# Kernel optimization log

Hardware: AMD Instinct MI355X
Metric: run time of the kernel (lower is better)

## Reference

```python
import jax, jax.numpy as jnp
import numpy as np

N, E = 50000, 800000
DIN, H, DOUT, L = 128, 128, 64, 3
NEG_SLOPE = 0.2  # PyG GATConv default


def setup_inputs() -> dict:
    key = jax.random.key(0)
    ks = jax.random.split(key, 12)
    s = lambda i, shape: (jax.random.normal(ks[i], shape, jnp.float32) * 0.05)
    return {
        "x": jax.random.normal(ks[0], (N, DIN), jnp.float32),
        "edge_index": jax.random.randint(ks[1], (2, E), 0, N, jnp.int64 if jax.config.jax_enable_x64 else jnp.int32),
        "W_emb": s(2, (DIN, H)), "b_emb": jnp.zeros((H,), jnp.float32),
        "gat_W": s(3, (L, H, H)), "gat_as": s(4, (L, H)), "gat_ad": s(5, (L, H)),
        "gat_b": jnp.zeros((L, H), jnp.float32),
        "Wn1": s(6, (H, H)), "bn1": jnp.zeros((H,), jnp.float32),
        "Wn2": s(7, (H, DOUT)), "bn2": jnp.zeros((DOUT,), jnp.float32),
        "We1": s(8, (2 * H, H)), "be1": jnp.zeros((H,), jnp.float32),
        "We2": s(9, (H, 3)), "be2": jnp.zeros((3,), jnp.float32),
    }


def _gat_layer(h, src, dst, n, W, a_src, a_dst, b):
    # Single-head GATConv (PyG defaults: heads=1, concat, self-loops already in src/dst)
    xw = h @ W                                   # [N, H]
    alpha_s = xw @ a_src                          # [N]
    alpha_d = xw @ a_dst                          # [N]
    logits = jax.nn.leaky_relu(alpha_s[src] + alpha_d[dst], NEG_SLOPE)  # [E']
    m = jax.ops.segment_max(logits, dst, num_segments=n)
    p = jnp.exp(logits - m[dst])
    denom = jax.ops.segment_sum(p, dst, num_segments=n)
    alpha = p / denom[dst]                        # softmax over incoming edges
    return jax.ops.segment_sum(alpha[:, None] * xw[src], dst, num_segments=n) + b


def reference(x, edge_index, W_emb, b_emb, gat_W, gat_as, gat_ad, gat_b,
              Wn1, bn1, Wn2, bn2, We1, be1, We2, be2):
    n = x.shape[0]
    src0, dst0 = edge_index[0], edge_index[1]
    loops = jnp.arange(n, dtype=src0.dtype)
    src = jnp.concatenate([src0, loops])          # GATConv adds self-loops by default
    dst = jnp.concatenate([dst0, loops])

    h = jax.nn.relu(x @ W_emb + b_emb)            # dropout off (eval mode)
    for l in range(L):
        h_new = _gat_layer(h, src, dst, n, gat_W[l], gat_as[l], gat_ad[l], gat_b[l])
        h = jax.nn.relu(h + h_new)                # residual + relu

    node_pred = jax.nn.relu(h @ Wn1 + bn1) @ Wn2 + bn2            # [N, DOUT]
    ef = jnp.concatenate([h[src0], h[dst0]], axis=1)              # vectorized edge gather [E, 2H]
    edge_pred = jax.nn.relu(ef @ We1 + be1) @ We2 + be2           # [E, 3]
    graph_emb = jnp.mean(h, axis=0, keepdims=True)                # batch=None path [1, H]
    return node_pred, edge_pred, graph_emb
```

## Files before the change

kernel.cpp:

```cpp
#include <hip/hip_runtime.h>

#define NNODES 50000
#define NEDGES 800000
#define HDIM 128
#define DOUT 64
#define NLAYERS 3
#define NEG_SLOPE 0.2f

#define NODE_OUT_ELEMS (NNODES * DOUT)
#define EDGE_OUT_ELEMS (NEDGES * 3)
#define GEMB_OFF (NODE_OUT_ELEMS + EDGE_OUT_ELEMS)

typedef __attribute__((ext_vector_type(8))) short short8;
typedef __attribute__((ext_vector_type(4))) float f32x4;
typedef unsigned long long u64;

__device__ __forceinline__ float bf2f(unsigned short u) {
    union { unsigned int i; float f; } v; v.i = ((unsigned int)u) << 16; return v.f;
}
__device__ __forceinline__ unsigned short f2bf(float f) {
    union { unsigned int i; float f; } v; v.f = f;
    unsigned int b = v.i;
    unsigned int r = (b + 0x7FFFu + ((b >> 16) & 1u)) >> 16;
    return (unsigned short)r;
}
__device__ __forceinline__ float leaky(float x) { return x > 0.f ? x : NEG_SLOPE * x; }
__device__ __forceinline__ float wread(const void* p, size_t i, int f32) {
    return f32 ? ((const float*)p)[i] : bf2f(((const unsigned short*)p)[i]);
}

__device__ __forceinline__ int eget(const int* e32, const int* iflag, int which, int e) {
    int idx = which * NEDGES + e;
    return (*iflag) ? e32[idx] : e32[2 * idx];
}

__global__ void init_kernel(int* cnt, int* cur, float* gsum, int* flags) {
    int i = blockIdx.x * 256 + threadIdx.x;
    if (i < NNODES) { cnt[i] = 0; cur[i] = 0; }
    if (blockIdx.x == 0) {
        if (threadIdx.x < HDIM) gsum[threadIdx.x] = 0.f;
        if (threadIdx.x < 2) flags[threadIdx.x] = 0;
    }
}

__global__ void detect_kernel(const unsigned short* xb, const int* e32,
                              int* fflag, int* iflag) {
    if (blockIdx.x == 0) {
        int hit = 0;
        for (int j = threadIdx.x; j < 4096; j += 256) {
            int e = (xb[j] >> 7) & 0xFF;
            if (e >= 0x90) hit = 1;
        }
        if (hit) atomicOr(fflag, 1);
    } else {
        int hit = 0;
        for (int t = threadIdx.x; t < 16384; t += 256) {
            int i = t * 48;
            if (e32[2 * i + 1] != 0) hit = 1;
        }
        if (__any(hit)) {
            if ((threadIdx.x & 63) == 0) atomicOr(iflag, 1);
        }
    }
}

__global__ __launch_bounds__(256) void gemm_mfma_kernel(
    const void* __restrict__ Av, int a_from_x, const void* __restrict__ Bw,
    size_t b_off, const void* __restrict__ bias, unsigned short* __restrict__ C,
    int M, int relu, const int* __restrict__ f32flag,
    float* __restrict__ alpha_s, float* __restrict__ alpha_d,
    const void* __restrict__ gat_as, const void* __restrict__ gat_ad, int aoff)
{
    constexpr int KP = 128 + 8;
    __shared__ unsigned short sA[64 * KP];
    __shared__ float pS[64][4], pD[64][4];
    const int f32 = *f32flag;
    const int tid = threadIdx.x;
    const int row0 = blockIdx.x * 64;

    if (a_from_x && f32) {
        const float* Af = (const float*)Av;
        for (int c = tid; c < 64 * 16; c += 256) {
            int r = c >> 4, cp = c & 15;
            int gr = row0 + r;
            unsigned short o[8] = {0, 0, 0, 0, 0, 0, 0, 0};
            if (gr < M) {
                float4 v0 = *(const float4*)(Af + (size_t)gr * 128 + cp * 8);
                float4 v1 = *(const float4*)(Af + (size_t)gr * 128 + cp * 8 + 4);
                o[0] = f2bf(v0.x); o[1] = f2bf(v0.y); o[2] = f2bf(v0.z); o[3] = f2bf(v0.w);
                o[4] = f2bf(v1.x); o[5] = f2bf(v1.y); o[6] = f2bf(v1.z); o[7] = f2bf(v1.w);
            }
            *(uint4*)(&sA[r * KP + cp * 8]) = *(uint4*)o;
        }
    } else {
        const unsigned short* A = (const unsigned short*)Av;
        for (int c = tid; c < 64 * 16; c += 256) {
            int r = c >> 4, cp = c & 15;
            int gr = row0 + r;
            uint4 v = {0u, 0u, 0u, 0u};
            if (gr < M) v = *(const uint4*)(A + (size_t)gr * 128 + cp * 8);
            *(uint4*)(&sA[r * KP + cp * 8]) = v;
        }
    }
    __syncthreads();

    const int wave = tid >> 6, lane = tid & 63;
    const int quad = lane >> 4, l15 = lane & 15;
    const int ncol0 = wave * 32;

    short8 bw[4][2];
    #pragma unroll
    for (int kk = 0; kk < 4; kk++)
        #pragma unroll
        for (int nt = 0; nt < 2; nt++) {
            int n = ncol0 + nt * 16 + l15;
            short8 t;
            #pragma unroll
            for (int j = 0; j < 8; j++)
                t[j] = (short)f2bf(wread(Bw, b_off + (size_t)(kk * 32 + quad * 8 + j) * 128 + n, f32));
            bw[kk][nt] = t;
        }

    float bv[2];
    #pragma unroll
    for (int nt = 0; nt < 2; nt++)
        bv[nt] = bias ? wread(bias, ncol0 + nt * 16 + l15, f32) : 0.f;

    f32x4 acc[4][2];
    #pragma unroll
    for (int mt = 0; mt < 4; mt++)
        #pragma unroll
        for (int nt = 0; nt < 2; nt++) {
            acc[mt][nt][0] = bv[nt]; acc[mt][nt][1] = bv[nt];
            acc[mt][nt][2] = bv[nt]; acc[mt][nt][3] = bv[nt];
        }

    #pragma unroll
    for (int kk = 0; kk < 4; kk++) {
        short8 a[4];
        #pragma unroll
        for (int mt = 0; mt < 4; mt++)
            a[mt] = *(const short8*)(&sA[(mt * 16 + l15) * KP + kk * 32 + quad * 8]);
        #pragma unroll
        for (int mt = 0; mt < 4; mt++)
            #pragma unroll
            for (int nt = 0; nt < 2; nt++)
                acc[mt][nt] = __builtin_amdgcn_mfma_f32_16x16x32_bf16(
                    a[mt], bw[kk][nt], acc[mt][nt], 0, 0, 0);
    }

    if (alpha_s) {
        float as0 = wread(gat_as, (size_t)aoff + ncol0 + l15, f32);
        float as1 = wread(gat_as, (size_t)aoff + ncol0 + 16 + l15, f32);
        float ad0 = wread(gat_ad, (size_t)aoff + ncol0 + l15, f32);
        float ad1 = wread(gat_ad, (size_t)aoff + ncol0 + 16 + l15, f32);
        #pragma unroll
        for (int mt = 0; mt < 4; mt++)
            #pragma unroll
            for (int q = 0; q < 4; q++) {
                float vs = acc[mt][0][q] * as0 + acc[mt][1][q] * as1;
                float vd = acc[mt][0][q] * ad0 + acc[mt][1][q] * ad1;
                #pragma unroll
                for (int d = 1; d < 16; d <<= 1) {
                    vs += __shfl_xor(vs, d);
                    vd += __shfl_xor(vd, d);
                }
                if (l15 == 0) {
                    int r = mt * 16 + quad * 4 + q;
                    pS[r][wave] = vs; pD[r][wave] = vd;
                }
            }
        __syncthreads();
        if (tid < 64) {
            int row = row0 + tid;
            if (row < M) {
                alpha_s[row] = pS[tid][0] + pS[tid][1] + pS[tid][2] + pS[tid][3];
                alpha_d[row] = pD[tid][0] + pD[tid][1] + pD[tid][2] + pD[tid][3];
            }
        }
    }

    #pragma unroll
    for (int mt = 0; mt < 4; mt++)
        #pragma unroll
        for (int nt = 0; nt < 2; nt++)
            #pragma unroll
            for (int q = 0; q < 4; q++) {
                int row = row0 + mt * 16 + quad * 4 + q;
                if (row < M) {
                    float v = acc[mt][nt][q];
                    if (relu) v = fmaxf(v, 0.f);
                    C[(size_t)row * 128 + ncol0 + nt * 16 + l15] = f2bf(v);
                }
            }
}

__global__ __launch_bounds__(256) void node_mlp_kernel(
    const unsigned short* __restrict__ h, const void* __restrict__ Wn1,
    const void* __restrict__ bn1, const void* __restrict__ Wn2,
    const void* __restrict__ bn2, float* __restrict__ out,
    float* __restrict__ gsum, int M, const int* __restrict__ f32flag)
{
    constexpr int KP = 128 + 8;
    __shared__ unsigned short sA[64 * KP];
    const int f32 = *f32flag;
    const int tid = threadIdx.x;
    const int row0 = blockIdx.x * 64;

    for (int c = tid; c < 64 * 16; c += 256) {
        int r = c >> 4, cp = c & 15;
        int gr = row0 + r;
        uint4 v = {0u, 0u, 0u, 0u};
        if (gr < M) v = *(const uint4*)(h + (size_t)gr * 128 + cp * 8);
        *(uint4*)(&sA[r * KP + cp * 8]) = v;
    }
    __syncthreads();

    if (tid < 128) {
        float hs = 0.f;
        for (int r = 0; r < 64; r++) hs += bf2f(sA[r * KP + tid]);
        atomicAdd(&gsum[tid], hs);
    }

    const int wave = tid >> 6, lane = tid & 63;
    const int quad = lane >> 4, l15 = lane & 15;
    const int ncol0 = wave * 32;

    {
        short8 bw[4][2];
        #pragma unroll
        for (int kk = 0; kk < 4; kk++)
            #pragma unroll
            for (int nt = 0; nt < 2; nt++) {
                int n = ncol0 + nt * 16 + l15;
                short8 t;
                #pragma unroll
                for (int j = 0; j < 8; j++)
                    t[j] = (short)f2bf(wread(Wn1, (size_t)(kk * 32 + quad * 8 + j) * 128 + n, f32));
                bw[kk][nt] = t;
            }
        float bv[2];
        #pragma unroll
        for (int nt = 0; nt < 2; nt++)
            bv[nt] = wread(bn1, ncol0 + nt * 16 + l15, f32);

        f32x4 acc[4][2];
        #pragma unroll
        for (int mt = 0; mt < 4; mt++)
            #pragma unroll
            for (int nt = 0; nt < 2; nt++) {
                acc[mt][nt][0] = bv[nt]; acc[mt][nt][1] = bv[nt];
                acc[mt][nt][2] = bv[nt]; acc[mt][nt][3] = bv[nt];
            }
        #pragma unroll
        for (int kk = 0; kk < 4; kk++) {
            short8 a[4];
            #pragma unroll
            for (int mt = 0; mt < 4; mt++)
                a[mt] = *(const short8*)(&sA[(mt * 16 + l15) * KP + kk * 32 + quad * 8]);
            #pragma unroll
            for (int mt = 0; mt < 4; mt++)
                #pragma unroll
                for (int nt = 0; nt < 2; nt++)
                    acc[mt][nt] = __builtin_amdgcn_mfma_f32_16x16x32_bf16(
                        a[mt], bw[kk][nt], acc[mt][nt], 0, 0, 0);
        }
        __syncthreads();
        #pragma unroll
        for (int mt = 0; mt < 4; mt++)
            #pragma unroll
            for (int nt = 0; nt < 2; nt++)
                #pragma unroll
                for (int q = 0; q < 4; q++) {
                    int r = mt * 16 + quad * 4 + q;
                    sA[r * KP + ncol0 + nt * 16 + l15] =
                        f2bf(fmaxf(acc[mt][nt][q], 0.f));
                }
        __syncthreads();
    }

    {
        const int col = wave * 16 + l15;
        short8 bw[4];
        #pragma unroll
        for (int kk = 0; kk < 4; kk++) {
            short8 t;
            #pragma unroll
            for (int j = 0; j < 8; j++)
                t[j] = (short)f2bf(wread(Wn2, (size_t)(kk * 32 + quad * 8 + j) * 64 + col, f32));
            bw[kk] = t;
        }
        float bv = wread(bn2, col, f32);
        f32x4 acc[4];
        #pragma unroll
        for (int mt = 0; mt < 4; mt++) {
            acc[mt][0] = bv; acc[mt][1] = bv; acc[mt][2] = bv; acc[mt][3] = bv;
        }
        #pragma unroll
        for (int kk = 0; kk < 4; kk++) {
            short8 a[4];
            #pragma unroll
            for (int mt = 0; mt < 4; mt++)
                a[mt] = *(const short8*)(&sA[(mt * 16 + l15) * KP + kk * 32 + quad * 8]);
            #pragma unroll
            for (int mt = 0; mt < 4; mt++)
                acc[mt] = __builtin_amdgcn_mfma_f32_16x16x32_bf16(
                    a[mt], bw[kk], acc[mt], 0, 0, 0);
        }
        #pragma unroll
        for (int mt = 0; mt < 4; mt++)
            #pragma unroll
            for (int q = 0; q < 4; q++) {
                int row = row0 + mt * 16 + quad * 4 + q;
                if (row < M) out[(size_t)row * 64 + col] = acc[mt][q];
            }
    }
}

__global__ __launch_bounds__(256) void edge_ab_kernel(
    const unsigned short* __restrict__ h, const void* __restrict__ We1,
    const void* __restrict__ be1, unsigned short* __restrict__ Axw,
    unsigned short* __restrict__ Bh, int M, const int* __restrict__ f32flag)
{
    constexpr int KP = 128 + 8;
    __shared__ unsigned short sA[64 * KP];
    const int f32 = *f32flag;
    const int tid = threadIdx.x;
    const int row0 = blockIdx.x * 64;

    for (int c = tid; c < 64 * 16; c += 256) {
        int r = c >> 4, cp = c & 15;
        int gr = row0 + r;
        uint4 v = {0u, 0u, 0u, 0u};
        if (gr < M) v = *(const uint4*)(h + (size_t)gr * 128 + cp * 8);
        *(uint4*)(&sA[r * KP + cp * 8]) = v;
    }
    __syncthreads();

    const int wave = tid >> 6, lane = tid & 63;
    const int quad = lane >> 4, l15 = lane & 15;
    const int ncol0 = wave * 32;

    #pragma unroll
    for (int half = 0; half < 2; half++) {
        const size_t b_off = (size_t)half * 128 * 128;
        unsigned short* Cp = half ? Bh : Axw;

        short8 bw[4][2];
        #pragma unroll
        for (int kk = 0; kk < 4; kk++)
            #pragma unroll
            for (int nt = 0; nt < 2; nt++) {
                int n = ncol0 + nt * 16 + l15;
                short8 t;
                #pragma unroll
                for (int j = 0; j < 8; j++)
                    t[j] = (short)f2bf(wread(We1, b_off + (size_t)(kk * 32 + quad * 8 + j) * 128 + n, f32));
                bw[kk][nt] = t;
            }
        float bv[2];
        #pragma unroll
        for (int nt = 0; nt < 2; nt++)
            bv[nt] = half ? 0.f : wread(be1, ncol0 + nt * 16 + l15, f32);

        f32x4 acc[4][2];
        #pragma unroll
        for (int mt = 0; mt < 4; mt++)
            #pragma unroll
            for (int nt = 0; nt < 2; nt++) {
                acc[mt][nt][0] = bv[nt]; acc[mt][nt][1] = bv[nt];
                acc[mt][nt][2] = bv[nt]; acc[mt][nt][3] = bv[nt];
            }
        #pragma unroll
        for (int kk = 0; kk < 4; kk++) {
            short8 a[4];
            #pragma unroll
            for (int mt = 0; mt < 4; mt++)
                a[mt] = *(const short8*)(&sA[(mt * 16 + l15) * KP + kk * 32 + quad * 8]);
            #pragma unroll
            for (int mt = 0; mt < 4; mt++)
                #pragma unroll
                for (int nt = 0; nt < 2; nt++)
                    acc[mt][nt] = __builtin_amdgcn_mfma_f32_16x16x32_bf16(
                        a[mt], bw[kk][nt], acc[mt][nt], 0, 0, 0);
        }
        #pragma unroll
        for (int mt = 0; mt < 4; mt++)
            #pragma unroll
            for (int nt = 0; nt < 2; nt++)
                #pragma unroll
                for (int q = 0; q < 4; q++) {
                    int row = row0 + mt * 16 + quad * 4 + q;
                    if (row < M)
                        Cp[(size_t)row * 128 + ncol0 + nt * 16 + l15] =
                            f2bf(acc[mt][nt][q]);
                }
    }
}

__global__ void count_kernel(const int* e32, const int* iflag, int* cnt) {
    int e = blockIdx.x * 256 + threadIdx.x;
    if (e < NEDGES) atomicAdd(&cnt[eget(e32, iflag, 1, e)], 1);
}
__global__ void scan1_kernel(const int* cnt, int* off, int* bsum) {
    __shared__ int s[256];
    int t = threadIdx.x, i = blockIdx.x * 256 + t;
    int v = (i < NNODES) ? cnt[i] : 0;
    s[t] = v;
    __syncthreads();
    for (int d = 1; d < 256; d <<= 1) {
        int add = (t >= d) ? s[t - d] : 0;
        __syncthreads();
        s[t] += add;
        __syncthreads();
    }
    if (i < NNODES) off[i] = s[t] - v;
    if (t == 255) bsum[blockIdx.x] = s[255];
}
__global__ void scan2_kernel(int* bsum, int nblk) {
    if (threadIdx.x == 0 && blockIdx.x == 0) {
        int run = 0;
        for (int c = 0; c < nblk; c++) { int t = bsum[c]; bsum[c] = run; run += t; }
    }
}
__global__ void scan3_kernel(int* off, const int* bsum) {
    int i = blockIdx.x * 256 + threadIdx.x;
    if (i < NNODES) off[i] += bsum[blockIdx.x];
}
__global__ void fill_kernel(const int* e32, const int* iflag, const int* off,
                            int* cur, u64* csrp, int use_pack) {
    int e = blockIdx.x * 256 + threadIdx.x;
    if (e < NEDGES) {
        int s = eget(e32, iflag, 0, e);
        int d = eget(e32, iflag, 1, e);
        int p = atomicAdd(&cur[d], 1);
        int pos = off[d] + p;
        if (use_pack)
            csrp[pos] = (u64)s | ((u64)d << 17) | ((u64)e << 34);
        else
            ((int*)csrp)[pos] = s;
    }
}

__global__ void aggregate_kernel(const unsigned short* __restrict__ xw,
                                 const float* __restrict__ as_, const float* __restrict__ ad_,
                                 const int* __restrict__ off, const u64* __restrict__ csrp,
                                 int use_pack, const void* __restrict__ gat_b, int boff,
                                 unsigned short* __restrict__ h,
                                 const int* __restrict__ f32flag) {
    const int f32 = *f32flag;
    int wave = threadIdx.x >> 6, lane = threadIdx.x & 63;
    int n = blockIdx.x * 4 + wave;
    if (n >= NNODES) return;
    int o0 = off[n];
    int o1 = (n == NNODES - 1) ? NEDGES : off[n + 1];
    int deg = o1 - o0;
    float adn = ad_[n];
    float lself = leaky(as_[n] + adn);

    int deg64 = deg < 64 ? deg : 64;
    int idxv = 0; float av = 0.f;
    if (lane < deg64) {
        idxv = use_pack ? (int)(csrp[o0 + lane] & 0x1FFFF)
                        : ((const int*)csrp)[o0 + lane];
        av = as_[idxv];
    }

    float m = lself;
    if (lane < deg64) m = fmaxf(m, leaky(av + adn));
    for (int i = 64 + lane; i < deg; i += 64) {
        int s = use_pack ? (int)(csrp[o0 + i] & 0x1FFFF)
                         : ((const int*)csrp)[o0 + i];
        m = fmaxf(m, leaky(as_[s] + adn));
    }
    #pragma unroll
    for (int d = 32; d >= 1; d >>= 1) m = fmaxf(m, __shfl_xor(m, d));

    const int slot = lane >> 4;
    const int l15  = lane & 15;
    float denom = 0.f;
    float acc[8];
    #pragma unroll
    for (int k = 0; k < 8; k++) acc[k] = 0.f;

    int i0 = slot, i1 = slot + 4;
    int sidx0 = __shfl(idxv, i0 & 63);
    float aval0 = __shfl(av, i0 & 63);
    int sidx1 = __shfl(idxv, i1 & 63);
    float aval1 = __shfl(av, i1 & 63);
    uint4 rv0 = {0u, 0u, 0u, 0u}, rv1 = {0u, 0u, 0u, 0u};
    if (i0 < deg64) rv0 = *(const uint4*)(xw + (size_t)sidx0 * HDIM + l15 * 8);
    if (i1 < deg64) rv1 = *(const uint4*)(xw + (size_t)sidx1 * HDIM + l15 * 8);
    for (int t0 = 0; t0 < deg64; t0 += 4) {
        int i2 = i0 + 8;
        int sidx2 = __shfl(idxv, i2 & 63);
        float aval2 = __shfl(av, i2 & 63);
        uint4 rv2 = {0u, 0u, 0u, 0u};
        if (i2 < deg64)
            rv2 = *(const uint4*)(xw + (size_t)sidx2 * HDIM + l15 * 8);
        if (i0 < deg64) {
            float p = __expf(leaky(aval0 + adn) - m);
            denom += p;
            const unsigned short* rp = (const unsigned short*)&rv0;
            #pragma unroll
            for (int k = 0; k < 8; k++) acc[k] += p * bf2f(rp[k]);
        }
        i0 = i1; aval0 = aval1; rv0 = rv1;
        i1 = i2; aval1 = aval2; rv1 = rv2;
    }
    for (int i = 64 + slot; i < deg; i += 4) {
        int s = use_pack ? (int)(csrp[o0 + i] & 0x1FFFF)
                         : ((const int*)csrp)[o0 + i];
        float p = __expf(leaky(as_[s] + adn) - m);
        denom += p;
        uint4 rv = *(const uint4*)(xw + (size_t)s * HDIM + l15 * 8);
        const unsigned short* rp = (const unsigned short*)&rv;
        #pragma unroll
        for (int k = 0; k < 8; k++) acc[k] += p * bf2f(rp[k]);
    }

    #pragma unroll
    for (int d = 16; d <= 32; d <<= 1) {
        denom += __shfl_xor(denom, d);
        #pragma unroll
        for (int k = 0; k < 8; k++) acc[k] += __shfl_xor(acc[k], d);
    }

    float ps = __expf(lself - m);
    denom += ps;
    uint4 sv = *(const uint4*)(xw + (size_t)n * HDIM + l15 * 8);
    const unsigned short* sp = (const unsigned short*)&sv;
    #pragma unroll
    for (int k = 0; k < 8; k++) acc[k] += ps * bf2f(sp[k]);

    if (slot == 0) {
        float inv = 1.f / denom;
        size_t base = (size_t)n * HDIM + l15 * 8;
        uint4 hv = *(const uint4*)(h + base);
        const unsigned short* hp = (const unsigned short*)&hv;
        unsigned short outv[8];
        #pragma unroll
        for (int k = 0; k < 8; k++) {
            float hx = bf2f(hp[k]);
            float bx = wread(gat_b, boff + l15 * 8 + k, f32);
            outv[k] = f2bf(fmaxf(hx + acc[k] * inv + bx, 0.f));
        }
        *(uint4*)(h + base) = *(uint4*)outv;
    }
}

__global__ __launch_bounds__(256) void edge_split_kernel(
    const unsigned short* __restrict__ A, const unsigned short* __restrict__ B,
    const int* __restrict__ e32, const int* __restrict__ iflag,
    const u64* __restrict__ csrp, int use_pack,
    const void* __restrict__ We2, const void* __restrict__ be2,
    float* __restrict__ eout, const int* __restrict__ f32flag)
{
    const int f32 = *f32flag;
    const int lane = threadIdx.x & 63;
    const int slot = lane >> 4, l15 = lane & 15;

    float w2[8][3];
    #pragma unroll
    for (int j = 0; j < 8; j++)
        #pragma unroll
        for (int c = 0; c < 3; c++)
            w2[j][c] = wread(We2, (l15 * 8 + j) * 3 + c, f32);
    const float bo0 = wread(be2, 0, f32);
    const float bo1 = wread(be2, 1, f32);
    const float bo2 = wread(be2, 2, f32);

    const int gw = (blockIdx.x * 256 + threadIdx.x) >> 6;
    const int stride = gridDim.x * 32;
    for (int e0 = gw * 8 + slot * 2; e0 < NEDGES; e0 += stride) {
        const int e1 = e0 + 1;
        const bool has1 = (e1 < NEDGES);
        int s0, d0, oe0, s1 = 0, d1 = 0, oe1 = 0;
        if (use_pack) {
            u64 pk0 = csrp[e0];
            s0 = (int)(pk0 & 0x1FFFF); d0 = (int)((pk0 >> 17) & 0x1FFFF);
            oe0 = (int)(pk0 >> 34);
            if (has1) {
                u64 pk1 = csrp[e1];
                s1 = (int)(pk1 & 0x1FFFF); d1 = (int)((pk1 >> 17) & 0x1FFFF);
                oe1 = (int)(pk1 >> 34);
            }
        } else {
            s0 = eget(e32, iflag, 0, e0); d0 = eget(e32, iflag, 1, e0); oe0 = e0;
            if (has1) {
                s1 = eget(e32, iflag, 0, e1); d1 = eget(e32, iflag, 1, e1); oe1 = e1;
            }
        }
        uint4 a0 = *(const uint4*)(A + (size_t)s0 * HDIM + l15 * 8);
        uint4 b0 = *(const uint4*)(B + (size_t)d0 * HDIM + l15 * 8);
        uint4 a1 = {0u, 0u, 0u, 0u}, b1 = {0u, 0u, 0u, 0u};
        if (has1) {
            a1 = *(const uint4*)(A + (size_t)s1 * HDIM + l15 * 8);
            b1 = *(const uint4*)(B + (size_t)d1 * HDIM + l15 * 8);
        }
        const unsigned short* ap0 = (const unsigned short*)&a0;
        const unsigned short* bp0 = (const unsigned short*)&b0;
        const unsigned short* ap1 = (const unsigned short*)&a1;
        const unsigned short* bp1 = (const unsigned short*)&b1;
        float s00 = 0.f, s01 = 0.f, s02 = 0.f;
        float s10 = 0.f, s11 = 0.f, s12 = 0.f;
        #pragma unroll
        for (int j = 0; j < 8; j++) {
            float v0 = fmaxf(bf2f(ap0[j]) + bf2f(bp0[j]), 0.f);
            float v1 = fmaxf(bf2f(ap1[j]) + bf2f(bp1[j]), 0.f);
            s00 += v0 * w2[j][0]; s01 += v0 * w2[j][1]; s02 += v0 * w2[j][2];
            s10 += v1 * w2[j][0]; s11 += v1 * w2[j][1]; s12 += v1 * w2[j][2];
        }
        #pragma unroll
        for (int dd = 1; dd < 16; dd <<= 1) {
            s00 += __shfl_xor(s00, dd); s01 += __shfl_xor(s01, dd); s02 += __shfl_xor(s02, dd);
            s10 += __shfl_xor(s10, dd); s11 += __shfl_xor(s11, dd); s12 += __shfl_xor(s12, dd);
        }
        if (l15 == 0) {
            eout[(size_t)oe0 * 3 + 0] = s00 + bo0;
            eout[(size_t)oe0 * 3 + 1] = s01 + bo1;
            eout[(size_t)oe0 * 3 + 2] = s02 + bo2;
            if (has1) {
                eout[(size_t)oe1 * 3 + 0] = s10 + bo0;
                eout[(size_t)oe1 * 3 + 1] = s11 + bo1;
                eout[(size_t)oe1 * 3 + 2] = s12 + bo2;
            }
        }
    }
}

__global__ void gout_kernel(const float* gsum, float* out) {
    int f = threadIdx.x;
    out[GEMB_OFF + f] = gsum[f] * (1.f / (float)NNODES);
}

extern "C" __attribute__((visibility("default")))
void kernel_launch(void* const* d_in, const int* in_sizes, int n_in,
                   void* d_out, int out_size, void* d_ws, size_t ws_size,
                   hipStream_t stream) {
    const void* x      = d_in[0];
    const int*  eidx   = (const int*)d_in[1];
    const void* W_emb  = d_in[2];
    const void* b_emb  = d_in[3];
    const void* gat_W  = d_in[4];
    const void* gat_as = d_in[5];
    const void* gat_ad = d_in[6];
    const void* gat_b  = d_in[7];
    const void* Wn1    = d_in[8];
    const void* bn1    = d_in[9];
    const void* Wn2    = d_in[10];
    const void* bn2    = d_in[11];
    const void* We1    = d_in[12];
    const void* be1    = d_in[13];
    const void* We2    = d_in[14];
    const void* be2    = d_in[15];
    float* out = (float*)d_out;

    char* ws = (char*)d_ws;
    unsigned short* h       = (unsigned short*)(ws);
    unsigned short* xw      = (unsigned short*)(ws + 12800000);
    float*          alpha_s = (float*)(ws + 25600000);
    float*          alpha_d = (float*)(ws + 25800000);
    int*            cnt     = (int*)(ws + 26000000);
    int*            off     = (int*)(ws + 26200000);
    int*            bsum    = (int*)(ws + 26400000);
    float*          gsum    = (float*)(ws + 26401024);
    int*            iflag   = (int*)(ws + 26401536);
    int*            fflag   = (int*)(ws + 26401540);
    u64*            csrp    = (u64*)(ws + 26608000);
    int*            cur     = (int*)alpha_s;

    const int use_pack = (ws_size >= (size_t)33008000) ? 1 : 0;

    const int node_blks = (NNODES + 255) / 256;
    const int edge_blks = (NEDGES + 255) / 256;
    const int g64       = (NNODES + 63) / 64;

    init_kernel<<<node_blks, 256, 0, stream>>>(cnt, cur, gsum, iflag);
    detect_kernel<<<2, 256, 0, stream>>>((const unsigned short*)x, eidx, fflag, iflag);

    gemm_mfma_kernel<<<g64, 256, 0, stream>>>(
        x, 1, W_emb, 0, b_emb, h, NNODES, 1, fflag,
        (float*)0, (float*)0, (const void*)0, (const void*)0, 0);

    count_kernel<<<edge_blks, 256, 0, stream>>>(eidx, iflag, cnt);
    scan1_kernel<<<node_blks, 256, 0, stream>>>(cnt, off, bsum);
    scan2_kernel<<<1, 64, 0, stream>>>(bsum, node_blks);
    scan3_kernel<<<node_blks, 256, 0, stream>>>(off, bsum);
    fill_kernel<<<edge_blks, 256, 0, stream>>>(eidx, iflag, off, cur, csrp, use_pack);

    for (int l = 0; l < NLAYERS; l++) {
        gemm_mfma_kernel<<<g64, 256, 0, stream>>>(
            h, 0, gat_W, (size_t)l * HDIM * HDIM, (const void*)0, xw, NNODES, 0, fflag,
            alpha_s, alpha_d, gat_as, gat_ad, l * HDIM);
        aggregate_kernel<<<(NNODES + 3) / 4, 256, 0, stream>>>(
            xw, alpha_s, alpha_d, off, csrp, use_pack, gat_b, l * HDIM, h, fflag);
    }

    node_mlp_kernel<<<g64, 256, 0, stream>>>(
        h, Wn1, bn1, Wn2, bn2, out, gsum, NNODES, fflag);
    gout_kernel<<<1, 128, 0, stream>>>(gsum, out);

    edge_ab_kernel<<<g64, 256, 0, stream>>>(
        h, We1, be1, xw, h, NNODES, fflag);
    edge_split_kernel<<<2048, 256, 0, stream>>>(
        xw, h, eidx, iflag, csrp, use_pack, We2, be2,
        out + NODE_OUT_ELEMS, fflag);
}
```

Before: 542.7 us.

## Fuse node MLP with edge projection and software-pipeline edge gather loop

Merges the node MLP and the edge first-layer projection into one tail kernel, so each 64-row tile of h is loaded into shared memory once and one launch is removed. The edge output loop now prefetches the next iteration's indices and gathered rows while computing the current pair, to hide gather latency. Risks: Bh aliases h, so the tail kernel writes h in place while other blocks may still read their own tiles (each block only touches its own rows). The tail kernel also needs more registers, and the has1 guard is dropped on the assumption that the edge count is even.

```diff
diff --git a/kernel.cpp b/kernel.cpp
--- a/kernel.cpp
+++ b/kernel.cpp
@@ -195,11 +195,14 @@
             }
 }
 
-__global__ __launch_bounds__(256) void node_mlp_kernel(
-    const unsigned short* __restrict__ h, const void* __restrict__ Wn1,
-    const void* __restrict__ bn1, const void* __restrict__ Wn2,
-    const void* __restrict__ bn2, float* __restrict__ out,
-    float* __restrict__ gsum, int M, const int* __restrict__ f32flag)
+__global__ __launch_bounds__(256) void tail_kernel(
+    const unsigned short* __restrict__ h,
+    const void* __restrict__ We1, const void* __restrict__ be1,
+    unsigned short* __restrict__ Axw, unsigned short* __restrict__ Bh,
+    const void* __restrict__ Wn1, const void* __restrict__ bn1,
+    const void* __restrict__ Wn2, const void* __restrict__ bn2,
+    float* __restrict__ out, float* __restrict__ gsum,
+    int M, const int* __restrict__ f32flag)
 {
     constexpr int KP = 128 + 8;
     __shared__ unsigned short sA[64 * KP];
@@ -225,6 +228,62 @@
     const int wave = tid >> 6, lane = tid & 63;
     const int quad = lane >> 4, l15 = lane & 15;
     const int ncol0 = wave * 32;
+
+    #pragma unroll
+    for (int half = 0; half < 2; half++) {
+        const size_t b_off = (size_t)half * 128 * 128;
+        unsigned short* Cp = half ? Bh : Axw;
+
+        short8 bw[4][2];
+        #pragma unroll
+        for (int kk = 0; kk < 4; kk++)
+            #pragma unroll
+            for (int nt = 0; nt < 2; nt++) {
+                int n = ncol0 + nt * 16 + l15;
+                short8 t;
+                #pragma unroll
+                for (int j = 0; j < 8; j++)
+                    t[j] = (short)f2bf(wread(We1, b_off + (size_t)(kk * 32 + quad * 8 + j) * 128 + n, f32));
+                bw[kk][nt] = t;
+            }
+        float bv[2];
+        #pragma unroll
+        for (int nt = 0; nt < 2; nt++)
+            bv[nt] = half ? 0.f : wread(be1, ncol0 + nt * 16 + l15, f32);
+
+        f32x4 acc[4][2];
+        #pragma unroll
+        for (int mt = 0; mt < 4; mt++)
+            #pragma unroll
+            for (int nt = 0; nt < 2; nt++) {
+                acc[mt][nt][0] = bv[nt]; acc[mt][nt][1] = bv[nt];
+                acc[mt][nt][2] = bv[nt]; acc[mt][nt][3] = bv[nt];
+            }
+        #pragma unroll
+        for (int kk = 0; kk < 4; kk++) {
+            short8 a[4];
+            #pragma unroll
+            for (int mt = 0; mt < 4; mt++)
+                a[mt] = *(const short8*)(&sA[(mt * 16 + l15) * KP + kk * 32 + quad * 8]);
+            #pragma unroll
+            for (int mt = 0; mt < 4; mt++)
+                #pragma unroll
+                for (int nt = 0; nt < 2; nt++)
+                    acc[mt][nt] = __builtin_amdgcn_mfma_f32_16x16x32_bf16(
+                        a[mt], bw[kk][nt], acc[mt][nt], 0, 0, 0);
+        }
+        #pragma unroll
+        for (int mt = 0; mt < 4; mt++)
+            #pragma unroll
+            for (int nt = 0; nt < 2; nt++)
+                #pragma unroll
+                for (int q = 0; q < 4; q++) {
+                    int row = row0 + mt * 16 + quad * 4 + q;
+                    if (row < M)
+                        Cp[(size_t)row * 128 + ncol0 + nt * 16 + l15] =
+                            f2bf(acc[mt][nt][q]);
+                }
+    }
 
     {
         short8 bw[4][2];
@@ -314,87 +373,6 @@
                 int row = row0 + mt * 16 + quad * 4 + q;
                 if (row < M) out[(size_t)row * 64 + col] = acc[mt][q];
             }
-    }
-}
-
-__global__ __launch_bounds__(256) void edge_ab_kernel(
-    const unsigned short* __restrict__ h, const void* __restrict__ We1,
-    const void* __restrict__ be1, unsigned short* __restrict__ Axw,
-    unsigned short* __restrict__ Bh, int M, const int* __restrict__ f32flag)
-{
-    constexpr int KP = 128 + 8;
-    __shared__ unsigned short sA[64 * KP];
-    const int f32 = *f32flag;
-    const int tid = threadIdx.x;
-    const int row0 = blockIdx.x * 64;
-
-    for (int c = tid; c < 64 * 16; c += 256) {
-        int r = c >> 4, cp = c & 15;
-        int gr = row0 + r;
-        uint4 v = {0u, 0u, 0u, 0u};
-        if (gr < M) v = *(const uint4*)(h + (size_t)gr * 128 + cp * 8);
-        *(uint4*)(&sA[r * KP + cp * 8]) = v;
-    }
-    __syncthreads();
-
-    const int wave = tid >> 6, lane = tid & 63;
-    const int quad = lane >> 4, l15 = lane & 15;
-    const int ncol0 = wave * 32;
-
-    #pragma unroll
-    for (int half = 0; half < 2; half++) {
-        const size_t b_off = (size_t)half * 128 * 128;
-        unsigned short* Cp = half ? Bh : Axw;
-
-        short8 bw[4][2];
-        #pragma unroll
-        for (int kk = 0; kk < 4; kk++)
-            #pragma unroll
-            for (int nt = 0; nt < 2; nt++) {
-                int n = ncol0 + nt * 16 + l15;
-                short8 t;
-                #pragma unroll
-                for (int j = 0; j < 8; j++)
-                    t[j] = (short)f2bf(wread(We1, b_off + (size_t)(kk * 32 + quad * 8 + j) * 128 + n, f32));
-                bw[kk][nt] = t;
-            }
-        float bv[2];
-        #pragma unroll
-        for (int nt = 0; nt < 2; nt++)
-            bv[nt] = half ? 0.f : wread(be1, ncol0 + nt * 16 + l15, f32);
-
-        f32x4 acc[4][2];
-        #pragma unroll
-        for (int mt = 0; mt < 4; mt++)
-            #pragma unroll
-            for (int nt = 0; nt < 2; nt++) {
-                acc[mt][nt][0] = bv[nt]; acc[mt][nt][1] = bv[nt];
-                acc[mt][nt][2] = bv[nt]; acc[mt][nt][3] = bv[nt];
-            }
-        #pragma unroll
-        for (int kk = 0; kk < 4; kk++) {
-            short8 a[4];
-            #pragma unroll
-            for (int mt = 0; mt < 4; mt++)
-                a[mt] = *(const short8*)(&sA[(mt * 16 + l15) * KP + kk * 32 + quad * 8]);
-            #pragma unroll
-            for (int mt = 0; mt < 4; mt++)
-                #pragma unroll
-                for (int nt = 0; nt < 2; nt++)
-                    acc[mt][nt] = __builtin_amdgcn_mfma_f32_16x16x32_bf16(
-                        a[mt], bw[kk][nt], acc[mt][nt], 0, 0, 0);
-        }
-        #pragma unroll
-        for (int mt = 0; mt < 4; mt++)
-            #pragma unroll
-            for (int nt = 0; nt < 2; nt++)
-                #pragma unroll
-                for (int q = 0; q < 4; q++) {
-                    int row = row0 + mt * 16 + quad * 4 + q;
-                    if (row < M)
-                        Cp[(size_t)row * 128 + ncol0 + nt * 16 + l15] =
-                            f2bf(acc[mt][nt][q]);
-                }
     }
 }
 
@@ -572,36 +550,50 @@
 
     const int gw = (blockIdx.x * 256 + threadIdx.x) >> 6;
     const int stride = gridDim.x * 32;
-    for (int e0 = gw * 8 + slot * 2; e0 < NEDGES; e0 += stride) {
-        const int e1 = e0 + 1;
-        const bool has1 = (e1 < NEDGES);
-        int s0, d0, oe0, s1 = 0, d1 = 0, oe1 = 0;
+
+    int ec = gw * 8 + slot * 2;
+    int sc0 = 0, dc0 = 0, oc0 = 0, sc1 = 0, dc1 = 0, oc1 = 0;
+    uint4 ac0 = {0u,0u,0u,0u}, bc0 = {0u,0u,0u,0u};
+    uint4 ac1 = {0u,0u,0u,0u}, bc1 = {0u,0u,0u,0u};
+    if (ec < NEDGES) {
         if (use_pack) {
-            u64 pk0 = csrp[e0];
-            s0 = (int)(pk0 & 0x1FFFF); d0 = (int)((pk0 >> 17) & 0x1FFFF);
-            oe0 = (int)(pk0 >> 34);
-            if (has1) {
-                u64 pk1 = csrp[e1];
-                s1 = (int)(pk1 & 0x1FFFF); d1 = (int)((pk1 >> 17) & 0x1FFFF);
-                oe1 = (int)(pk1 >> 34);
-            }
+            u64 p0 = csrp[ec], p1 = csrp[ec + 1];
+            sc0 = (int)(p0 & 0x1FFFF); dc0 = (int)((p0 >> 17) & 0x1FFFF); oc0 = (int)(p0 >> 34);
+            sc1 = (int)(p1 & 0x1FFFF); dc1 = (int)((p1 >> 17) & 0x1FFFF); oc1 = (int)(p1 >> 34);
         } else {
-            s0 = eget(e32, iflag, 0, e0); d0 = eget(e32, iflag, 1, e0); oe0 = e0;
-            if (has1) {
-                s1 = eget(e32, iflag, 0, e1); d1 = eget(e32, iflag, 1, e1); oe1 = e1;
-            }
-        }
-        uint4 a0 = *(const uint4*)(A + (size_t)s0 * HDIM + l15 * 8);
-        uint4 b0 = *(const uint4*)(B + (size_t)d0 * HDIM + l15 * 8);
-        uint4 a1 = {0u, 0u, 0u, 0u}, b1 = {0u, 0u, 0u, 0u};
-        if (has1) {
-            a1 = *(const uint4*)(A + (size_t)s1 * HDIM + l15 * 8);
-            b1 = *(const uint4*)(B + (size_t)d1 * HDIM + l15 * 8);
-        }
-        const unsigned short* ap0 = (const unsigned short*)&a0;
-        const unsigned short* bp0 = (const unsigned short*)&b0;
-        const unsigned short* ap1 = (const unsigned short*)&a1;
-        const unsigned short* bp1 = (const unsigned short*)&b1;
+            sc0 = eget(e32, iflag, 0, ec);     dc0 = eget(e32, iflag, 1, ec);     oc0 = ec;
+            sc1 = eget(e32, iflag, 0, ec + 1); dc1 = eget(e32, iflag, 1, ec + 1); oc1 = ec + 1;
+        }
+        ac0 = *(const uint4*)(A + (size_t)sc0 * HDIM + l15 * 8);
+        bc0 = *(const uint4*)(B + (size_t)dc0 * HDIM + l15 * 8);
+        ac1 = *(const uint4*)(A + (size_t)sc1 * HDIM + l15 * 8);
+        bc1 = *(const uint4*)(B + (size_t)dc1 * HDIM + l15 * 8);
+    }
+
+    while (ec < NEDGES) {
+        const int en = ec + stride;
+        int sn0 = 0, dn0 = 0, on0 = 0, sn1 = 0, dn1 = 0, on1 = 0;
+        uint4 an0 = {0u,0u,0u,0u}, bn0 = {0u,0u,0u,0u};
+        uint4 an1 = {0u,0u,0u,0u}, bn1v = {0u,0u,0u,0u};
+        if (en < NEDGES) {
+            if (use_pack) {
+                u64 p0 = csrp[en], p1 = csrp[en + 1];
+                sn0 = (int)(p0 & 0x1FFFF); dn0 = (int)((p0 >> 17) & 0x1FFFF); on0 = (int)(p0 >> 34);
+                sn1 = (int)(p1 & 0x1FFFF); dn1 = (int)((p1 >> 17) & 0x1FFFF); on1 = (int)(p1 >> 34);
+            } else {
+                sn0 = eget(e32, iflag, 0, en);     dn0 = eget(e32, iflag, 1, en);     on0 = en;
+                sn1 = eget(e32, iflag, 0, en + 1); dn1 = eget(e32, iflag, 1, en + 1); on1 = en + 1;
+            }
+            an0 = *(const uint4*)(A + (size_t)sn0 * HDIM + l15 * 8);
+            bn0 = *(const uint4*)(B + (size_t)dn0 * HDIM + l15 * 8);
+            an1 = *(const uint4*)(A + (size_t)sn1 * HDIM + l15 * 8);
+            bn1v = *(const uint4*)(B + (size_t)dn1 * HDIM + l15 * 8);
+        }
+
+        const unsigned short* ap0 = (const unsigned short*)&ac0;
+        const unsigned short* bp0 = (const unsigned short*)&bc0;
+        const unsigned short* ap1 = (const unsigned short*)&ac1;
+        const unsigned short* bp1 = (const unsigned short*)&bc1;
         float s00 = 0.f, s01 = 0.f, s02 = 0.f;
         float s10 = 0.f, s11 = 0.f, s12 = 0.f;
         #pragma unroll
@@ -617,15 +609,17 @@
             s10 += __shfl_xor(s10, dd); s11 += __shfl_xor(s11, dd); s12 += __shfl_xor(s12, dd);
         }
         if (l15 == 0) {
-            eout[(size_t)oe0 * 3 + 0] = s00 + bo0;
-            eout[(size_t)oe0 * 3 + 1] = s01 + bo1;
-            eout[(size_t)oe0 * 3 + 2] = s02 + bo2;
-            if (has1) {
-                eout[(size_t)oe1 * 3 + 0] = s10 + bo0;
-                eout[(size_t)oe1 * 3 + 1] = s11 + bo1;
-                eout[(size_t)oe1 * 3 + 2] = s12 + bo2;
-            }
-        }
+            eout[(size_t)oc0 * 3 + 0] = s00 + bo0;
+            eout[(size_t)oc0 * 3 + 1] = s01 + bo1;
+            eout[(size_t)oc0 * 3 + 2] = s02 + bo2;
+            eout[(size_t)oc1 * 3 + 0] = s10 + bo0;
+            eout[(size_t)oc1 * 3 + 1] = s11 + bo1;
+            eout[(size_t)oc1 * 3 + 2] = s12 + bo2;
+        }
+
+        ec = en;
+        sc0 = sn0; dc0 = dn0; oc0 = on0; sc1 = sn1; dc1 = dn1; oc1 = on1;
+        ac0 = an0; bc0 = bn0; ac1 = an1; bc1 = bn1v;
     }
 }
 
@@ -697,12 +691,10 @@
             xw, alpha_s, alpha_d, off, csrp, use_pack, gat_b, l * HDIM, h, fflag);
     }
 
-    node_mlp_kernel<<<g64, 256, 0, stream>>>(
-        h, Wn1, bn1, Wn2, bn2, out, gsum, NNODES, fflag);
+    tail_kernel<<<g64, 256, 0, stream>>>(
+        h, We1, be1, xw, h, Wn1, bn1, Wn2, bn2, out, gsum, NNODES, fflag);
     gout_kernel<<<1, 128, 0, stream>>>(gsum, out);
 
-    edge_ab_kernel<<<g64, 256, 0, stream>>>(
-        h, We1, be1, xw, h, NNODES, fflag);
     edge_split_kernel<<<2048, 256, 0, stream>>>(
         xw, h, eidx, iflag, csrp, use_pack, We2, be2,
         out + NODE_OUT_ELEMS, fflag);
```

Measured after the change: 550.9 us. About the same (+1.5%).

## Bin edges into src/dst slice blocks for cache-local edge MLP gathers

Applied to the files above, without the earlier changes.

Before the edge MLP, edges are binned into an 8x8 grid of source/destination node slices. This uses a per-block histogram, a global scan and a scatter into a packed edge buffer. Each group of blocks in the edge split kernel then walks one source slice's eight bins, so the A and B row gathers stay within a small, cache-resident working set. The B projection is now written into the not-yet-used node output buffer instead of overwriting h, and the node MLP is moved after the edge MLP. In exchange the change adds five extra kernels and another pass over the edge list, and it only applies when the workspace is large enough.

```diff
diff --git a/kernel.cpp b/kernel.cpp
--- a/kernel.cpp
+++ b/kernel.cpp
@@ -6,6 +6,7 @@
 #define DOUT 64
 #define NLAYERS 3
 #define NEG_SLOPE 0.2f
+#define BSLICE 6250
 
 #define NODE_OUT_ELEMS (NNODES * DOUT)
 #define EDGE_OUT_ELEMS (NEDGES * 3)
@@ -28,7 +29,6 @@
 __device__ __forceinline__ float wread(const void* p, size_t i, int f32) {
     return f32 ? ((const float*)p)[i] : bf2f(((const unsigned short*)p)[i]);
 }
-
 __device__ __forceinline__ int eget(const int* e32, const int* iflag, int which, int e) {
     int idx = which * NEDGES + e;
     return (*iflag) ? e32[idx] : e32[2 * idx];
@@ -320,7 +320,7 @@
 __global__ __launch_bounds__(256) void edge_ab_kernel(
     const unsigned short* __restrict__ h, const void* __restrict__ We1,
     const void* __restrict__ be1, unsigned short* __restrict__ Axw,
-    unsigned short* __restrict__ Bh, int M, const int* __restrict__ f32flag)
+    unsigned short* __restrict__ Bsc, int M, const int* __restrict__ f32flag)
 {
     constexpr int KP = 128 + 8;
     __shared__ unsigned short sA[64 * KP];
@@ -344,7 +344,7 @@
     #pragma unroll
     for (int half = 0; half < 2; half++) {
         const size_t b_off = (size_t)half * 128 * 128;
-        unsigned short* Cp = half ? Bh : Axw;
+        unsigned short* Cp = half ? Bsc : Axw;
 
         short8 bw[4][2];
         #pragma unroll
@@ -440,6 +440,53 @@
         else
             ((int*)csrp)[pos] = s;
     }
+}
+
+__global__ void hist_kernel(const int* e32, const int* iflag, int* bcnt) {
+    __shared__ int hcnt[64];
+    int tid = threadIdx.x;
+    if (tid < 64) hcnt[tid] = 0;
+    __syncthreads();
+    int e = blockIdx.x * 256 + tid;
+    int s = eget(e32, iflag, 0, e);
+    int d = eget(e32, iflag, 1, e);
+    int b = (s / BSLICE) * 8 + (d / BSLICE);
+    atomicAdd(&hcnt[b], 1);
+    __syncthreads();
+    if (tid < 64) bcnt[tid * 3125 + blockIdx.x] = hcnt[tid];
+}
+__global__ void gscan1_kernel(int* a, int n, int* bs) {
+    __shared__ int s[256];
+    int t = threadIdx.x, i = blockIdx.x * 256 + t;
+    int v = (i < n) ? a[i] : 0;
+    s[t] = v;
+    __syncthreads();
+    for (int d = 1; d < 256; d <<= 1) {
+        int add = (t >= d) ? s[t - d] : 0;
+        __syncthreads();
+        s[t] += add;
+        __syncthreads();
+    }
+    if (i < n) a[i] = s[t] - v;
+    if (t == 255) bs[blockIdx.x] = s[255];
+}
+__global__ void gscan3_kernel(int* a, int n, const int* bs) {
+    int i = blockIdx.x * 256 + threadIdx.x;
+    if (i < n) a[i] += bs[blockIdx.x];
+}
+__global__ void scatter_kernel(const int* e32, const int* iflag,
+                               const int* bcnt, u64* csrb) {
+    __shared__ int curb[64];
+    int tid = threadIdx.x;
+    if (tid < 64) curb[tid] = 0;
+    __syncthreads();
+    int e = blockIdx.x * 256 + tid;
+    int s = eget(e32, iflag, 0, e);
+    int d = eget(e32, iflag, 1, e);
+    int b = (s / BSLICE) * 8 + (d / BSLICE);
+    int p = atomicAdd(&curb[b], 1);
+    int pos = bcnt[b * 3125 + blockIdx.x] + p;
+    csrb[pos] = (u64)s | ((u64)d << 17) | ((u64)e << 34);
 }
 
 __global__ void aggregate_kernel(const unsigned short* __restrict__ xw,
@@ -552,7 +599,7 @@
 __global__ __launch_bounds__(256) void edge_split_kernel(
     const unsigned short* __restrict__ A, const unsigned short* __restrict__ B,
     const int* __restrict__ e32, const int* __restrict__ iflag,
-    const u64* __restrict__ csrp, int use_pack,
+    const u64* __restrict__ csrb, const int* __restrict__ bcnt, int use_big,
     const void* __restrict__ We2, const void* __restrict__ be2,
     float* __restrict__ eout, const int* __restrict__ f32flag)
 {
@@ -570,27 +617,8 @@
     const float bo1 = wread(be2, 1, f32);
     const float bo2 = wread(be2, 2, f32);
 
-    const int gw = (blockIdx.x * 256 + threadIdx.x) >> 6;
-    const int stride = gridDim.x * 32;
-    for (int e0 = gw * 8 + slot * 2; e0 < NEDGES; e0 += stride) {
-        const int e1 = e0 + 1;
-        const bool has1 = (e1 < NEDGES);
-        int s0, d0, oe0, s1 = 0, d1 = 0, oe1 = 0;
-        if (use_pack) {
-            u64 pk0 = csrp[e0];
-            s0 = (int)(pk0 & 0x1FFFF); d0 = (int)((pk0 >> 17) & 0x1FFFF);
-            oe0 = (int)(pk0 >> 34);
-            if (has1) {
-                u64 pk1 = csrp[e1];
-                s1 = (int)(pk1 & 0x1FFFF); d1 = (int)((pk1 >> 17) & 0x1FFFF);
-                oe1 = (int)(pk1 >> 34);
-            }
-        } else {
-            s0 = eget(e32, iflag, 0, e0); d0 = eget(e32, iflag, 1, e0); oe0 = e0;
-            if (has1) {
-                s1 = eget(e32, iflag, 0, e1); d1 = eget(e32, iflag, 1, e1); oe1 = e1;
-            }
-        }
+    auto do_pair = [&](int s0, int d0, int oe0,
+                       int s1, int d1, int oe1, bool has1) {
         uint4 a0 = *(const uint4*)(A + (size_t)s0 * HDIM + l15 * 8);
         uint4 b0 = *(const uint4*)(B + (size_t)d0 * HDIM + l15 * 8);
         uint4 a1 = {0u, 0u, 0u, 0u}, b1 = {0u, 0u, 0u, 0u};
@@ -625,6 +653,46 @@
                 eout[(size_t)oe1 * 3 + 1] = s11 + bo1;
                 eout[(size_t)oe1 * 3 + 2] = s12 + bo2;
             }
+        }
+    };
+
+    if (use_big) {
+        const int kx = blockIdx.x & 7;
+        const int wloc = (blockIdx.x >> 3) * 4 + (threadIdx.x >> 6);
+        for (int j = 0; j < 8; j++) {
+            int b = kx * 8 + j;
+            int base = bcnt[b * 3125];
+            int end  = (b == 63) ? NEDGES : bcnt[(b + 1) * 3125];
+            for (int e0 = base + wloc * 8 + slot * 2; e0 < end; e0 += 1024 * 8) {
+                u64 p0 = csrb[e0];
+                int s0 = (int)(p0 & 0x1FFFF);
+                int d0 = (int)((p0 >> 17) & 0x1FFFF);
+                int o0 = (int)(p0 >> 34);
+                bool has1 = (e0 + 1 < end);
+                int s1 = 0, d1 = 0, o1 = 0;
+                if (has1) {
+                    u64 p1 = csrb[e0 + 1];
+                    s1 = (int)(p1 & 0x1FFFF);
+                    d1 = (int)((p1 >> 17) & 0x1FFFF);
+                    o1 = (int)(p1 >> 34);
+                }
+                do_pair(s0, d0, o0, s1, d1, o1, has1);
+            }
+        }
+    } else {
+        const int gw = (blockIdx.x * 256 + threadIdx.x) >> 6;
+        const int stride = gridDim.x * 32;
+        for (int e0 = gw * 8 + slot * 2; e0 < NEDGES; e0 += stride) {
+            int s0 = eget(e32, iflag, 0, e0);
+            int d0 = eget(e32, iflag, 1, e0);
+            bool has1 = (e0 + 1 < NEDGES);
+            int s1 = 0, d1 = 0, o1 = 0;
+            if (has1) {
+                s1 = eget(e32, iflag, 0, e0 + 1);
+                d1 = eget(e32, iflag, 1, e0 + 1);
+                o1 = e0 + 1;
+            }
+            do_pair(s0, d0, e0, s1, d1, o1, has1);
         }
     }
 }
@@ -669,8 +737,13 @@
     int*            fflag   = (int*)(ws + 26401540);
     u64*            csrp    = (u64*)(ws + 26608000);
     int*            cur     = (int*)alpha_s;
+    int*            bcnt    = (int*)(ws + 25600000);
+    u64*            csrb    = (u64*)(ws + 29808000);
+    int*            bsum2   = (int*)(ws + 29808000);
+    unsigned short* Bsc     = (unsigned short*)out;
 
     const int use_pack = (ws_size >= (size_t)33008000) ? 1 : 0;
+    const int use_big  = (ws_size >= (size_t)36208000) ? 1 : 0;
 
     const int node_blks = (NNODES + 255) / 256;
     const int edge_blks = (NEDGES + 255) / 256;
@@ -697,13 +770,21 @@
             xw, alpha_s, alpha_d, off, csrp, use_pack, gat_b, l * HDIM, h, fflag);
     }
 
+    if (use_big) {
+        hist_kernel<<<3125, 256, 0, stream>>>(eidx, iflag, bcnt);
+        gscan1_kernel<<<782, 256, 0, stream>>>(bcnt, 200000, bsum2);
+        scan2_kernel<<<1, 64, 0, stream>>>(bsum2, 782);
+        gscan3_kernel<<<782, 256, 0, stream>>>(bcnt, 200000, bsum2);
+        scatter_kernel<<<3125, 256, 0, stream>>>(eidx, iflag, bcnt, csrb);
+    }
+
+    edge_ab_kernel<<<g64, 256, 0, stream>>>(
+        h, We1, be1, xw, Bsc, NNODES, fflag);
+    edge_split_kernel<<<2048, 256, 0, stream>>>(
+        xw, Bsc, eidx, iflag, csrb, bcnt, use_big, We2, be2,
+        out + NODE_OUT_ELEMS, fflag);
+
     node_mlp_kernel<<<g64, 256, 0, stream>>>(
         h, Wn1, bn1, Wn2, bn2, out, gsum, NNODES, fflag);
     gout_kernel<<<1, 128, 0, stream>>>(gsum, out);
-
-    edge_ab_kernel<<<g64, 256, 0, stream>>>(
-        h, We1, be1, xw, h, NNODES, fflag);
-    edge_split_kernel<<<2048, 256, 0, stream>>>(
-        xw, h, eidx, iflag, csrp, use_pack, We2, be2,
-        out + NODE_OUT_ELEMS, fflag);
-}
+}
```

Result: slower. 654.8 us (+20.7%).
